# Optimization experiments

Hardware: AMD Instinct MI355X
Metric: run time of the kernel (lower is better)

Reference implementation:

```python
import jax, jax.numpy as jnp
import numpy as np

# dims: batch, n_sentences, n_comments, embedding_dim(==latent_dim), k
B, NS, NC, D, K = 16, 1024, 1024, 128, 128
K_CONV = 128.0   # curvature passed to poincare<->lorentz conversions (forward uses curv = self.k)
K_MAN = 1.0      # Lorentz manifold curvature (curv=1.0)
MIN_NORM = 1e-15


def p2l(x, k):
    # geoopt lmath.poincare_to_lorentz: dim d -> d+1
    x2 = jnp.sum(x * x, axis=-1, keepdims=True)
    return jnp.sqrt(k) * jnp.concatenate([1.0 + x2, 2.0 * x], axis=-1) / (1.0 - x2 + 1e-6)


def l2p(x, k):
    # geoopt lmath.lorentz_to_poincare: dim d+1 -> d
    return x[..., 1:] / (x[..., :1] + jnp.sqrt(k))


def lorentz_linear(x, W, b, log_scale):
    # HyboNet-style LorentzLinear: euclidean linear then rescale space so time^2 - |space|^2 = 1
    y = x @ W.T + b
    time = jax.nn.sigmoid(y[..., :1]) * jnp.exp(log_scale) + 1.1
    space = y[..., 1:]
    s2 = jnp.clip(jnp.sum(space * space, axis=-1, keepdims=True), 1e-8, None)
    return jnp.concatenate([time, space * jnp.sqrt((time * time - 1.0) / s2)], axis=-1)


def lorentz_tanh(x):
    # LorentzAct(tanh): tanh on space components, recompute time on the k=1 hyperboloid
    space = jnp.tanh(x[..., 1:])
    time = jnp.sqrt(K_MAN + jnp.sum(space * space, axis=-1, keepdims=True))
    return jnp.concatenate([time, space], axis=-1)


def artanh(x):
    return jnp.arctanh(jnp.clip(x, -1.0 + 1e-5, 1.0 - 1e-5))


def mobius_scale(mx, x_norm):
    # geoopt mobius_matvec (c=1) given the plain matrix product mx and the input row norms
    mx_norm = jnp.clip(jnp.linalg.norm(mx, axis=-1, keepdims=True), MIN_NORM, None)
    return jnp.tanh(mx_norm / x_norm * artanh(x_norm)) * mx / mx_norm


def mobius_add(x, y):
    # geoopt mobius_add, c=1
    xy = jnp.sum(x * y, axis=-1, keepdims=True)
    x2 = jnp.sum(x * x, axis=-1, keepdims=True)
    y2 = jnp.sum(y * y, axis=-1, keepdims=True)
    num = (1.0 + 2.0 * xy + y2) * x + (1.0 - x2) * y
    return num / jnp.clip(1.0 + 2.0 * xy + x2 * y2, MIN_NORM, None)


def lorentz_centroid(w, x):
    # CustomLorentz.centroid: weighted sum projected back to the hyperboloid
    avg = jnp.einsum('bqn,bnd->bqd', w, x)
    inner = jnp.sum(avg[..., 1:] ** 2, axis=-1, keepdims=True) - avg[..., :1] ** 2  # <avg,avg>_L
    return jnp.sqrt(K_MAN) * avg / jnp.sqrt(jnp.clip(jnp.abs(inner), 1e-8, None))


def setup_inputs() -> dict:
    key = jax.random.key(0)
    ks = jax.random.split(key, 8)

    def ball(k_, shape):
        # points safely inside the unit Poincare ball (norm ~ 0.58)
        u = jax.random.uniform(k_, shape, jnp.float32, minval=-1.0, maxval=1.0)
        return u / jnp.sqrt(jnp.float32(shape[-1]))

    def lin(k_, din, dout):
        kw, kb = jax.random.split(k_)
        W = jax.random.normal(kw, (dout, din), jnp.float32) * jnp.float32(1.0 / np.sqrt(din))
        b = jax.random.normal(kb, (dout,), jnp.float32) * 0.01
        return W, b

    Wl_w, Wl_b = lin(ks[2], D + 1, D + 1)
    Ws_w, Ws_b = lin(ks[3], D + 1, K + 1)
    Wc_w, Wc_b = lin(ks[4], D + 1, K + 1)
    return {
        'sentence_rep': ball(ks[0], (B, NS, D)),
        'comment_rep': ball(ks[1], (B, NC, D)),
        'Wl_w': Wl_w, 'Wl_b': Wl_b, 'Wl_scale': jnp.float32(np.log(10.0)),
        'Ws_w': Ws_w, 'Ws_b': Ws_b, 'Ws_scale': jnp.float32(np.log(10.0)),
        'Wc_w': Wc_w, 'Wc_b': Wc_b, 'Wc_scale': jnp.float32(np.log(10.0)),
        'whs': jax.random.normal(ks[5], (1, K + 1), jnp.float32),
        'whc': jax.random.normal(ks[6], (1, K + 1), jnp.float32),
    }


def reference(sentence_rep, comment_rep, Wl_w, Wl_b, Wl_scale, Ws_w, Ws_b, Ws_scale,
              Wc_w, Wc_b, Wc_scale, whs, whc):
    ls = p2l(sentence_rep, K_CONV)                       # [B,NS,D+1]
    lc = p2l(comment_rep, K_CONV)                        # [B,NC,D+1]

    Lw = lorentz_linear(lc, Wl_w, Wl_b, Wl_scale)        # [B,NC,D+1]
    L = lorentz_tanh(jnp.einsum('bsd,bcd->bsc', ls, Lw)) # [B,NS,NC] affinity

    Ps = l2p(lorentz_linear(ls, Ws_w, Ws_b, Ws_scale), K_CONV)  # [B,NS,K]
    Pc = l2p(lorentz_linear(lc, Wc_w, Wc_b, Wc_scale), K_CONV)  # [B,NC,K]

    Ln = jnp.clip(jnp.linalg.norm(L, axis=-1, keepdims=True), MIN_NORM, None)      # row norms of L
    LTn = jnp.clip(jnp.linalg.norm(L, axis=-2), MIN_NORM, None)[..., None]         # row norms of L^T

    Hs = lorentz_tanh(p2l(mobius_add(Ps, mobius_scale(jnp.einsum('bsc,bck->bsk', L, Pc), Ln)), K_CONV))   # [B,NS,K+1]
    Hc = lorentz_tanh(p2l(mobius_add(Pc, mobius_scale(jnp.einsum('bsc,bsk->bck', L, Ps), LTn)), K_CONV))  # [B,NC,K+1]

    Hs_n = jnp.clip(jnp.linalg.norm(Hs, axis=-1, keepdims=True), MIN_NORM, None)
    Hc_n = jnp.clip(jnp.linalg.norm(Hc, axis=-1, keepdims=True), MIN_NORM, None)
    As = jax.nn.softmax(mobius_scale(jnp.einsum('bnk,ok->bno', Hs, whs), Hs_n).swapaxes(-1, -2), axis=-1)  # [B,1,NS]
    Ac = jax.nn.softmax(mobius_scale(jnp.einsum('bnk,ok->bno', Hc, whc), Hc_n).swapaxes(-1, -2), axis=-1)  # [B,1,NC]

    co_s = lorentz_centroid(As, ls)                      # [B,1,D+1]
    co_c = lorentz_centroid(Ac, lc)                      # [B,1,D+1]

    # Lorentz direct concat: concat space parts, recompute time
    space = jnp.concatenate([co_s[..., 1:], co_c[..., 1:]], axis=-1)
    time = jnp.sqrt(K_MAN + jnp.sum(space * space, axis=-1, keepdims=True))
    co_sc = jnp.concatenate([time, space], axis=-1)[:, 0, :]  # squeeze -> [B,2D+1]
    return co_sc, As, Ac
```

## Files before the change

### kernel.cpp

```cpp
#include <hip/hip_runtime.h>

#define NN 1024
#define NB 16
#define SQRTK 11.313708498984761f

typedef float f32x4 __attribute__((ext_vector_type(4)));
typedef short bf16x8 __attribute__((ext_vector_type(8)));
typedef unsigned short ushort_t;
typedef unsigned int uint_t;

__device__ __forceinline__ ushort_t f2bf(float f){
  uint_t u = __float_as_uint(f);
  u += 0x7fffu + ((u>>16)&1u);
  return (ushort_t)(u>>16);
}
__device__ __forceinline__ float bf2f(ushort_t h){ return __uint_as_float(((uint_t)h)<<16); }

__device__ __forceinline__ uint_t cvtpk_bf16(float a, float b){
  uint_t r;
  asm("v_cvt_pk_bf16_f32 %0, %1, %2" : "=v"(r) : "v"(a), "v"(b));
  return r;
}

__device__ __forceinline__ float fast_tanh(float x){
  float e = __expf(2.f*x);
  return 1.f - 2.f/(e+1.f);
}

__device__ __forceinline__ float artanh_clip(float x){
  x = fminf(fmaxf(x, -1.0f+1e-5f), 1.0f-1e-5f);
  return 0.5f*__logf((1.0f+x)/(1.0f-x));
}

__device__ __forceinline__ void stage_swz(const ushort_t* __restrict__ g, int row_stride,
                                          char* ldsbase, int nrows, int tid, int nw){
  int lane = tid & 63;
  int w = tid >> 6;
  int ninst = nrows >> 2;
  int r_in = lane >> 4;
  int s_in = lane & 15;
  for (int inst = w; inst < ninst; inst += nw){
    int r = (inst<<2) + r_in;
    int s = s_in ^ (r & 15);
    const ushort_t* src = g + (size_t)r*row_stride + (s<<3);
    int instU = __builtin_amdgcn_readfirstlane(inst);
    __builtin_amdgcn_global_load_lds((const __attribute__((address_space(1))) void*)src,
        (__attribute__((address_space(3))) void*)(ldsbase + (instU<<10)), 16, 0, 0);
  }
}

__device__ __forceinline__ bf16x8 ldsfrag(const char* base, int r, int slot){
  return *(const bf16x8*)(base + ((r<<8) + ((slot ^ (r&15))<<4)));
}

__global__ void k_p2l(const float* __restrict__ S, const float* __restrict__ C,
                      ushort_t* __restrict__ lsb, ushort_t* __restrict__ lcb,
                      float* __restrict__ lst, float* __restrict__ lct,
                      const float* __restrict__ Wl, const float* __restrict__ Ws,
                      const float* __restrict__ Wc, ushort_t* __restrict__ Wb,
                      float* __restrict__ Wt){
  if (blockIdx.x >= 8192){
    int gid = (blockIdx.x - 8192)*256 + threadIdx.x;
    int w = gid / 18432;
    int rem = gid - w*18432;
    int j = rem >> 7, col = rem & 127;
    const float* W = (w==0)? Wl : (w==1? Ws : Wc);
    float v;
    if (j < 128) v = W[j*129 + 1 + col];
    else if (j == 128) v = W[128*129 + 1 + col];
    else v = 0.f;
    Wb[(size_t)w*18432 + (j<<7) + col] = f2bf(v);
    if (col==0 && j<=128) Wt[w*132 + j] = W[j*129];
    return;
  }
  int gr = (blockIdx.x<<2) + (threadIdx.x>>6);
  int lane = threadIdx.x & 63;
  const float* in; ushort_t* ob; float* ot;
  if (gr < (NB<<10)){ in = S + (size_t)gr*128; ob = lsb + (size_t)gr*128; ot = lst+gr; }
  else { int r = gr - (NB<<10); in = C + (size_t)r*128; ob = lcb + (size_t)r*128; ot = lct+r; }
  float2 v = ((const float2*)in)[lane];
  float sq = v.x*v.x + v.y*v.y;
  #pragma unroll
  for (int o=32;o>0;o>>=1) sq += __shfl_xor(sq, o, 64);
  float inv = SQRTK/(1.f - sq + 1e-6f);
  uint_t pack = (uint_t)f2bf(2.f*v.x*inv) | ((uint_t)f2bf(2.f*v.y*inv)<<16);
  ((uint_t*)ob)[lane] = pack;
  if (lane==0) *ot = (1.f+sq)*inv;
}

__global__ __launch_bounds__(256) void k_linf(
    const ushort_t* __restrict__ lsb, const ushort_t* __restrict__ lcb,
    const float* __restrict__ lst, const float* __restrict__ lct,
    const ushort_t* __restrict__ Wb, const float* __restrict__ Wt,
    const float* __restrict__ bl, const float* __restrict__ bs, const float* __restrict__ bc,
    const float* __restrict__ scl, const float* __restrict__ scs, const float* __restrict__ scc,
    ushort_t* __restrict__ Lwb, float* __restrict__ Lwt,
    ushort_t* __restrict__ Psb, ushort_t* __restrict__ Pcb,
    ushort_t* __restrict__ PsT, ushort_t* __restrict__ PcT){
  __shared__ __attribute__((aligned(1024))) char Al[16*1024];
  __shared__ __attribute__((aligned(1024))) char Bl[33*1024];
  __shared__ float XtF[64];
  __shared__ float wtsh[128];
  __shared__ float bsh[129];
  __shared__ float y128sh[64];
  __shared__ float y0sh[64];
  __shared__ float red2[64][2];
  __shared__ float facsh[64];
  int which = blockIdx.y;
  int m0 = blockIdx.x << 6;
  const ushort_t* A = ((which==1)? lsb : lcb) + (size_t)m0*128;
  const float* At = ((which==1)? lst : lct) + m0;
  const ushort_t* B = Wb + (size_t)which*18432;
  const float* bias = (which==0)? bl : (which==1? bs : bc);
  float scale = __expf((which==0)? *scl : (which==1? *scs : *scc));
  int tid = threadIdx.x, lane = tid&63, w = tid>>6;
  int wr = w>>1, wc = w&1, lo = lane&15, hi = lane>>4;
  stage_swz(A, 128, Al, 64, tid, 4);
  stage_swz(B, 128, Bl, 132, tid, 4);
  if (tid < 64) XtF[tid] = At[tid];
  if (tid < 128) wtsh[tid] = Wt[which*132 + tid];
  for (int i2 = tid; i2 < 129; i2 += 256) bsh[i2] = bias[i2];
  __syncthreads();
  f32x4 acc[2][4];
  f32x4 acc5[2];
  #pragma unroll
  for (int i=0;i<2;i++){
    acc5[i] = (f32x4){0.f,0.f,0.f,0.f};
    #pragma unroll
    for (int q=0;q<4;q++) acc[i][q] = (f32x4){0.f,0.f,0.f,0.f};
  }
  #pragma unroll
  for (int kc=0; kc<4; ++kc){
    bf16x8 av[2], bv[4];
    #pragma unroll
    for (int i=0;i<2;i++) av[i] = ldsfrag(Al, (wr<<5)+(i<<4)+lo, (kc<<2)+hi);
    #pragma unroll
    for (int q=0;q<4;q++) bv[q] = ldsfrag(Bl, (wc<<6)+(q<<4)+lo, (kc<<2)+hi);
    #pragma unroll
    for (int i=0;i<2;i++)
      #pragma unroll
      for (int q=0;q<4;q++)
        acc[i][q] = __builtin_amdgcn_mfma_f32_16x16x32_bf16(av[i], bv[q], acc[i][q], 0,0,0);
    if (wc==0){
      bf16x8 bv5 = ldsfrag(Bl, 128 + (lo&3), (kc<<2)+hi);
      #pragma unroll
      for (int i=0;i<2;i++)
        acc5[i] = __builtin_amdgcn_mfma_f32_16x16x32_bf16(av[i], bv5, acc5[i], 0,0,0);
    }
  }
  if (wc==0 && lo==0){
    #pragma unroll
    for (int i=0;i<2;i++)
      #pragma unroll
      for (int j=0;j<4;j++)
        y128sh[(wr<<5)+(i<<4)+(hi<<2)+j] = acc5[i][j];
  }
  float s2p[2][4];
  #pragma unroll
  for (int i=0;i<2;i++)
    #pragma unroll
    for (int j=0;j<4;j++) s2p[i][j] = 0.f;
  #pragma unroll
  for (int i=0;i<2;i++){
    f32x4 xt4 = *(const f32x4*)&XtF[(wr<<5)+(i<<4)+(hi<<2)];
    #pragma unroll
    for (int q=0;q<4;q++){
      int cl = (wc<<6)+(q<<4)+lo;
      float wtv = wtsh[cl];
      float bvv = bsh[cl];
      #pragma unroll
      for (int j=0;j<4;j++){
        float y = acc[i][q][j] + xt4[j]*wtv + bvv;
        acc[i][q][j] = y;
        if (cl==0){ y0sh[(wr<<5)+(i<<4)+(hi<<2)+j] = y; }
        else s2p[i][j] += y*y;
      }
    }
  }
  #pragma unroll
  for (int i=0;i<2;i++)
    #pragma unroll
    for (int j=0;j<4;j++){
      float v = s2p[i][j];
      v += __shfl_xor(v,1,64); v += __shfl_xor(v,2,64);
      v += __shfl_xor(v,4,64); v += __shfl_xor(v,8,64);
      s2p[i][j] = v;
    }
  if (lo==0){
    #pragma unroll
    for (int i=0;i<2;i++)
      #pragma unroll
      for (int j=0;j<4;j++) red2[(wr<<5)+(i<<4)+(hi<<2)+j][wc] = s2p[i][j];
  }
  __syncthreads();
  if (tid < 64){
    float wt128t = Wt[which*132 + 128];
    float y128v = y128sh[tid] + XtF[tid]*wt128t + bsh[128];
    y128sh[tid] = y128v;
    float s2 = fmaxf(red2[tid][0]+red2[tid][1] + y128v*y128v, 1e-8f);
    float y0 = y0sh[tid];
    float time = scale/(1.f+__expf(-y0)) + 1.1f;
    float fac = sqrtf((time*time-1.f)/s2);
    float iv = (which==0)? fac : fac/(time+SQRTK);
    facsh[tid] = iv;
    if (which==0) Lwt[m0+tid] = time;
  }
  __syncthreads();
  ushort_t* T2 = (ushort_t*)Bl;
  ushort_t* Ob = ((which==0)? Lwb : (which==1? Psb : Pcb)) + (size_t)m0*128;
  #pragma unroll
  for (int i=0;i<2;i++){
    f32x4 fv = *(const f32x4*)&facsh[(wr<<5)+(i<<4)+(hi<<2)];
    #pragma unroll
    for (int q=0;q<4;q++){
      int cl = (wc<<6)+(q<<4)+lo;
      if (cl > 0){
        #pragma unroll
        for (int j=0;j<4;j++){
          int row = (wr<<5)+(i<<4)+(hi<<2)+j;
          ushort_t v16 = f2bf(acc[i][q][j]*fv[j]);
          Ob[(size_t)row*128 + (cl-1)] = v16;
          if (which) T2[(cl-1)*68 + row] = v16;
        }
      }
    }
  }
  if (tid < 64){
    ushort_t v16 = f2bf(y128sh[tid]*facsh[tid]);
    Ob[(size_t)tid*128 + 127] = v16;
    if (which) T2[127*68 + tid] = v16;
  }
  if (which){
    __syncthreads();
    int b = m0 >> 10, n0 = m0 & 1023;
    ushort_t* PT = ((which==1)? PsT : PcT) + ((size_t)b<<17) + n0;
    for (int idx = tid; idx < 2048; idx += 256){
      int k = idx >> 4, seg = idx & 15;
      uint2 v = *(const uint2*)&T2[k*68 + (seg<<2)];
      *(uint2*)(PT + (size_t)k*1024 + (seg<<2)) = v;
    }
  }
}

__global__ __launch_bounds__(512) void k_fused(
    const ushort_t* __restrict__ lsb, const float* __restrict__ lst,
    const ushort_t* __restrict__ Lwb, const float* __restrict__ Lwt,
    const ushort_t* __restrict__ PsT, const ushort_t* __restrict__ PcT,
    const ushort_t* __restrict__ Pcb,
    float* __restrict__ mxs, float* __restrict__ mxc,
    float* __restrict__ Ln, float* __restrict__ LTn, float* __restrict__ tv){
  __shared__ __attribute__((aligned(1024))) char Rres[16*1024];
  __shared__ __attribute__((aligned(1024))) char STbuf[32*1024];
  __shared__ __attribute__((aligned(1024))) char Pbuf[16*1024];
  __shared__ float RtF[64];
  __shared__ float StF[128];
  __shared__ float pc0[128];
  __shared__ float red[64][4];
  __shared__ float tvsh[64];
  int side = blockIdx.y;
  int bx = blockIdx.x;
  bx = ((bx & 7) << 5) + (bx >> 3);
  int b = bx >> 4;
  int r0 = (bx & 15) << 6;
  const ushort_t* Rb = (side? Lwb : lsb) + ((size_t)((b<<10) + r0))*128;
  const float*    Rt = (side? Lwt : lst) + (b<<10) + r0;
  const ushort_t* Sb = (side? lsb : Lwb) + ((size_t)(b<<10))*128;
  const float*    St = (side? lst : Lwt) + (b<<10);
  const ushort_t* Tb = (side? PsT : PcT) + ((size_t)b<<17);
  float* C = (side? mxc : mxs) + ((size_t)((b<<10) + r0))*128;
  int tid = threadIdx.x, lane = tid&63, w = tid>>6;
  int lo = lane&15, hi = lane>>4;
  int wS = w>>1, wR = w&1;
  int wm = w&1, wn = w>>1;
  f32x4 acc2[2][2];
  #pragma unroll
  for (int i=0;i<2;i++)
    #pragma unroll
    for (int q=0;q<2;q++) acc2[i][q] = (f32x4){0.f,0.f,0.f,0.f};
  float tpart[2] = {0.f, 0.f};
  stage_swz(Rb, 128, Rres, 64, tid, 8);
  if (tid < 64) RtF[tid] = Rt[tid];
  if (tid < 128) pc0[tid] = side ? 0.f : bf2f(Pcb[((size_t)(b<<10))*128 + tid]);
  for (int ct=0; ct<8; ++ct){
    int s0 = ct<<7;
    __syncthreads();
    stage_swz(Sb + (size_t)s0*128, 128, STbuf, 128, tid, 8);
    if (tid < 128) StF[tid] = St[s0 + tid];
    __syncthreads();
    f32x4 d[2][2];
    #pragma unroll
    for (int i=0;i<2;i++)
      #pragma unroll
      for (int q=0;q<2;q++) d[i][q] = (f32x4){0.f,0.f,0.f,0.f};
    #pragma unroll
    for (int kc=0;kc<4;kc++){
      bf16x8 av[2], bv[2];
      #pragma unroll
      for (int i=0;i<2;i++) av[i] = ldsfrag(STbuf, (wS<<5)+(i<<4)+lo, (kc<<2)+hi);
      #pragma unroll
      for (int q=0;q<2;q++) bv[q] = ldsfrag(Rres, (wR<<5)+(q<<4)+lo, (kc<<2)+hi);
      #pragma unroll
      for (int i=0;i<2;i++)
        #pragma unroll
        for (int q=0;q<2;q++)
          d[i][q] = __builtin_amdgcn_mfma_f32_16x16x32_bf16(av[i], bv[q], d[i][q], 0,0,0);
    }
    __syncthreads();
    stage_swz(Tb + s0, 1024, STbuf, 128, tid, 8);
    #pragma unroll
    for (int i=0;i<2;i++){
      int st4 = (wS<<5)+(i<<4)+(hi<<2);
      f32x4 stv = *(const f32x4*)&StF[st4];
      #pragma unroll
      for (int q=0;q<2;q++){
        int rs = (wR<<5)+(q<<4)+lo;
        float rt = RtF[rs];
        float tval[4];
        #pragma unroll
        for (int j=0;j<4;j++){
          float val = d[i][q][j] + stv[j]*rt;
          bool dead = side ? ((r0+rs)==0) : ((s0+st4+j)==0);
          float tvv = fast_tanh(val);
          tvv = dead ? 0.f : tvv;
          tpart[q] += tvv*tvv;
          tval[j] = tvv;
        }
        uint2 pw;
        pw.x = cvtpk_bf16(tval[0], tval[1]);
        pw.y = cvtpk_bf16(tval[2], tval[3]);
        *(uint2*)(Pbuf + (rs<<8) + ((((st4>>3)^(rs&15)))<<4) + ((st4&7)<<1)) = pw;
      }
    }
    __syncthreads();
    #pragma unroll
    for (int kc=0;kc<4;kc++){
      bf16x8 av2[2], bv2[2];
      #pragma unroll
      for (int i=0;i<2;i++) av2[i] = ldsfrag(Pbuf, (wm<<5)+(i<<4)+lo, (kc<<2)+hi);
      #pragma unroll
      for (int q=0;q<2;q++) bv2[q] = ldsfrag(STbuf, (wn<<5)+(q<<4)+lo, (kc<<2)+hi);
      #pragma unroll
      for (int i=0;i<2;i++)
        #pragma unroll
        for (int q=0;q<2;q++)
          acc2[i][q] = __builtin_amdgcn_mfma_f32_16x16x32_bf16(av2[i], bv2[q], acc2[i][q], 0,0,0);
    }
  }
  #pragma unroll
  for (int q=0;q<2;q++){
    tpart[q] += __shfl_xor(tpart[q], 16, 64);
    tpart[q] += __shfl_xor(tpart[q], 32, 64);
  }
  if (hi==0){
    #pragma unroll
    for (int q=0;q<2;q++) red[(wR<<5)+(q<<4)+lo][w>>1] = tpart[q];
  }
  __syncthreads();
  if (tid < 64){
    float T = red[tid][0]+red[tid][1]+red[tid][2]+red[tid][3];
    int g = (b<<10) + r0 + tid;
    if (side==0){
      float timev = sqrtf(1.f+T);
      tvsh[tid] = timev;
      tv[g] = timev;
      Ln[g] = sqrtf(1.f+2.f*T);
    } else {
      if ((r0+tid) != 0) LTn[g] = fmaxf(sqrtf(T), 1e-15f);
      tvsh[tid] = 0.f;
    }
  }
  __syncthreads();
  #pragma unroll
  for (int i=0;i<2;i++){
    int rr4 = (wm<<5)+(i<<4)+(hi<<2);
    f32x4 tvv = *(const f32x4*)&tvsh[rr4];
    #pragma unroll
    for (int q=0;q<2;q++){
      int k = (wn<<5)+(q<<4)+lo;
      float p0 = pc0[k];
      #pragma unroll
      for (int j=0;j<4;j++){
        float v = acc2[i][q][j];
        if (side==0) v += tvv[j]*p0;
        C[(size_t)(rr4+j)*128 + k] = v;
      }
    }
  }
}

__global__ void k_fix2(const float* __restrict__ tv, const ushort_t* __restrict__ Psb,
                       float* __restrict__ mxc, float* __restrict__ LTn){
  __shared__ float tvl[1024];
  __shared__ float fpar[8][128];
  __shared__ float red16[16];
  int b = blockIdx.x, t = threadIdx.x;
  float v = tv[(b<<10)+t];
  tvl[t] = v;
  float sq = v*v;
  #pragma unroll
  for (int o=32;o>0;o>>=1) sq += __shfl_xor(sq,o,64);
  if ((t&63)==0) red16[t>>6] = sq;
  __syncthreads();
  int ch = t>>7, k = t&127;
  const ushort_t* P = Psb + (((size_t)(b<<10)) + (ch<<7))*128;
  const float* tc = &tvl[ch<<7];
  float acc = 0.f;
  #pragma unroll 4
  for (int s=0; s<128; ++s) acc += tc[s]*bf2f(P[(size_t)s*128 + k]);
  fpar[ch][k] = acc;
  __syncthreads();
  if (t < 128){
    float a = 0.f;
    #pragma unroll
    for (int c2=0; c2<8; ++c2) a += fpar[c2][t];
    mxc[((size_t)(b<<10))*128 + t] = a;
  }
  if (t == 0){
    float s = 0.f;
    #pragma unroll
    for (int c2=0; c2<16; ++c2) s += red16[c2];
    LTn[b<<10] = fmaxf(sqrtf(s), 1e-15f);
  }
}

__global__ __launch_bounds__(256) void k_epi(const float* __restrict__ mxs,
    const float* __restrict__ mxc,
    const ushort_t* __restrict__ Psb, const ushort_t* __restrict__ Pcb,
    const float* __restrict__ Ln, const float* __restrict__ LTn,
    const float* __restrict__ whs, const float* __restrict__ whc, float* __restrict__ logit){
  int wid = threadIdx.x >> 6, lane = threadIdx.x & 63;
  int gr = (blockIdx.x << 2) + wid;
  int side = gr >> 14, row = gr & 16383;
  const float* mx = (side? mxc : mxs) + (size_t)row*128;
  const ushort_t* xP = (side? Pcb : Psb) + (size_t)row*128;
  float xn = (side? LTn : Ln)[row];
  const float* wh = side? whc : whs;
  float2 mv = ((const float2*)mx)[lane];
  uint_t xu = ((const uint_t*)xP)[lane];
  float x0 = bf2f((ushort_t)(xu & 0xffffu));
  float x1 = bf2f((ushort_t)(xu >> 16));
  float pa = mv.x*mv.x + mv.y*mv.y;
  float pb = x0*x0 + x1*x1;
  float pc = x0*mv.x + x1*mv.y;
  #pragma unroll
  for (int o=32;o>0;o>>=1){
    pa += __shfl_xor(pa,o,64);
    pb += __shfl_xor(pb,o,64);
    pc += __shfl_xor(pc,o,64);
  }
  float mxn = fmaxf(sqrtf(pa), 1e-15f);
  float at1 = artanh_clip(xn);
  float fac = fast_tanh(mxn/xn*at1)/mxn;
  float xy = fac*pc;
  float x2 = pb;
  float y2 = fac*fac*pa;
  float den = fmaxf(1.0f + 2.0f*xy + x2*y2, 1e-15f);
  float ca = (1.0f+2.0f*xy+y2)/den;
  float cb = (1.0f-x2)*fac/den;
  float ma0 = ca*x0 + cb*mv.x;
  float ma1 = ca*x1 + cb*mv.y;
  float pm = ma0*ma0 + ma1*ma1;
  #pragma unroll
  for (int o=32;o>0;o>>=1) pm += __shfl_xor(pm,o,64);
  float scal = SQRTK*2.0f/(1.0f - pm + 1e-6f);
  float h0 = fast_tanh(scal*ma0);
  float h1 = fast_tanh(scal*ma1);
  float wv0 = wh[1 + 2*lane];
  float wv1 = wh[2 + 2*lane];
  float ps = h0*h0 + h1*h1;
  float pd = h0*wv0 + h1*wv1;
  #pragma unroll
  for (int o=32;o>0;o>>=1){
    ps += __shfl_xor(ps,o,64);
    pd += __shfl_xor(pd,o,64);
  }
  float timev = sqrtf(1.0f + ps);
  float hn = fmaxf(sqrtf(1.0f + 2.0f*ps), 1e-15f);
  float dotv = pd + timev*wh[0];
  float at2 = artanh_clip(hn);
  float mn = fmaxf(fabsf(dotv), 1e-15f);
  float lg = fast_tanh(mn/hn*at2)*(dotv/mn);
  if (lane==0) logit[gr] = lg;
}

__global__ void k_softmax(const float* __restrict__ logit,
                          float* __restrict__ outAs, float* __restrict__ outAc){
  __shared__ float red4[4];
  int side = blockIdx.x >> 4;
  int b = blockIdx.x & 15;
  const float* lg = logit + (side<<14) + (b<<10);
  float* out = (side? outAc : outAs) + (b<<10);
  int t = threadIdx.x;
  float l[4]; float m = -1e30f;
  #pragma unroll
  for (int i=0;i<4;i++){ l[i] = lg[t+256*i]; m = fmaxf(m,l[i]); }
  #pragma unroll
  for (int o=32;o>0;o>>=1) m = fmaxf(m, __shfl_xor(m,o,64));
  if ((t&63)==0) red4[t>>6]=m;
  __syncthreads();
  m = fmaxf(fmaxf(red4[0],red4[1]), fmaxf(red4[2],red4[3]));
  __syncthreads();
  float s = 0.f; float e[4];
  #pragma unroll
  for (int i=0;i<4;i++){ e[i] = __expf(l[i]-m); s += e[i]; }
  #pragma unroll
  for (int o=32;o>0;o>>=1) s += __shfl_xor(s,o,64);
  if ((t&63)==0) red4[t>>6]=s;
  __syncthreads();
  s = red4[0]+red4[1]+red4[2]+red4[3];
  float invs = 1.0f/s;
  #pragma unroll
  for (int i=0;i<4;i++) out[t+256*i] = e[i]*invs;
}

__global__ void k_cpart(const float* __restrict__ As0, const float* __restrict__ Ac0,
    const ushort_t* __restrict__ lsb, const ushort_t* __restrict__ lcb,
    const float* __restrict__ lst, const float* __restrict__ lct, float* __restrict__ part){
  __shared__ float Psh[64];
  __shared__ float ppar[128];
  int ch = blockIdx.x, b = blockIdx.y, side = blockIdx.z;
  const float* P = (side? Ac0 : As0) + (b<<10) + (ch<<6);
  const ushort_t* Xb = (side? lcb : lsb) + (((size_t)(b<<10)) + (ch<<6))*128;
  const float* Xt = (side? lct : lst) + (b<<10) + (ch<<6);
  int t = threadIdx.x;
  if (t < 64) Psh[t] = P[t];
  __syncthreads();
  int col = t & 127, half = t >> 7;
  float acc = 0.f;
  int n0 = half<<5;
  #pragma unroll 4
  for (int n=n0; n<n0+32; ++n) acc += Psh[n]*bf2f(Xb[(size_t)n*128 + col]);
  if (half==1) ppar[col] = acc;
  float acct = 0.f;
  if (t==255){
    for (int n=0;n<64;++n) acct += Psh[n]*Xt[n];
  }
  __syncthreads();
  size_t base = ((((size_t)side<<4) + b)*16 + ch)*132;
  if (t < 128) part[base + t] = acc + ppar[t];
  if (t == 255) part[base + 128] = acct;
}

__global__ void k_cfin2(const float* __restrict__ part, float* __restrict__ out){
  __shared__ float red4[4];
  __shared__ float t0sh;
  __shared__ float csh[2][128];
  int b = blockIdx.x, t = threadIdx.x;
  for (int side=0; side<2; ++side){
    int sb = side*16 + b;
    float a = 0.f;
    if (t <= 128){
      #pragma unroll
      for (int ch=0; ch<16; ++ch) a += part[((size_t)sb*16+ch)*132 + t];
    }
    float val = (t < 128)? a*a : 0.f;
    #pragma unroll
    for (int o=32;o>0;o>>=1) val += __shfl_xor(val,o,64);
    __syncthreads();
    if ((t&63)==0) red4[t>>6]=val;
    if (t==128) t0sh = a;
    __syncthreads();
    float S = red4[0]+red4[1]+red4[2]+red4[3];
    float timev = t0sh;
    float dn = sqrtf(fmaxf(fabsf(S - timev*timev), 1e-8f));
    if (t < 128) csh[side][t] = a/dn;
  }
  __syncthreads();
  float sp = (t<128)? csh[0][t] : csh[1][t-128];
  float v = sp*sp;
  #pragma unroll
  for (int o=32;o>0;o>>=1) v += __shfl_xor(v,o,64);
  __syncthreads();
  if ((t&63)==0) red4[t>>6]=v;
  __syncthreads();
  float S = red4[0]+red4[1]+red4[2]+red4[3];
  float* ob = out + (size_t)b*257;
  if (t==0) ob[0] = sqrtf(1.0f + S);
  ob[1+t] = sp;
}

extern "C" void kernel_launch(void* const* d_in, const int* in_sizes, int n_in,
                              void* d_out, int out_size, void* d_ws, size_t ws_size,
                              hipStream_t stream) {
  const float* srep = (const float*)d_in[0];
  const float* crep = (const float*)d_in[1];
  const float* Wl_w = (const float*)d_in[2];
  const float* Wl_b = (const float*)d_in[3];
  const float* Wl_s = (const float*)d_in[4];
  const float* Ws_w = (const float*)d_in[5];
  const float* Ws_b = (const float*)d_in[6];
  const float* Ws_s = (const float*)d_in[7];
  const float* Wc_w = (const float*)d_in[8];
  const float* Wc_b = (const float*)d_in[9];
  const float* Wc_s = (const float*)d_in[10];
  const float* whs  = (const float*)d_in[11];
  const float* whc  = (const float*)d_in[12];
  float* out = (float*)d_out;

  char* wsb = (char*)d_ws;
  size_t off = 0;
  auto alloc = [&](size_t n)->char*{ char* p = wsb + off; off += (n + 255) & ~(size_t)255; return p; };
  ushort_t* lsb = (ushort_t*)alloc((size_t)16384*128*2);
  ushort_t* lcb = (ushort_t*)alloc((size_t)16384*128*2);
  float* lst = (float*)alloc(16384*4);
  float* lct = (float*)alloc(16384*4);
  ushort_t* Wb = (ushort_t*)alloc((size_t)3*18432*2);
  float* Wt = (float*)alloc(3*132*4);
  ushort_t* Lwb = (ushort_t*)alloc((size_t)16384*128*2);
  float* Lwt = (float*)alloc(16384*4);
  ushort_t* Psb = (ushort_t*)alloc((size_t)16384*128*2);
  ushort_t* Pcb = (ushort_t*)alloc((size_t)16384*128*2);
  ushort_t* PsT = (ushort_t*)alloc((size_t)16*128*1024*2);
  ushort_t* PcT = (ushort_t*)alloc((size_t)16*128*1024*2);
  float* mxs = (float*)alloc((size_t)16384*128*4);
  float* mxc = (float*)alloc((size_t)16384*128*4);
  float* Ln = (float*)alloc(16384*4);
  float* LTn = (float*)alloc(16384*4);
  float* tv = (float*)alloc(16384*4);
  float* logit = (float*)alloc((size_t)2*16384*4);
  float* part = (float*)alloc((size_t)2*16*16*132*4);

  float* outAs = out + NB*257;
  float* outAc = out + NB*257 + NB*NN;

  k_p2l<<<8408, 256, 0, stream>>>(srep, crep, lsb, lcb, lst, lct,
                                  Wl_w, Ws_w, Wc_w, Wb, Wt);
  k_linf<<<dim3(256,3), 256, 0, stream>>>(lsb, lcb, lst, lct, Wb, Wt,
                                          Wl_b, Ws_b, Wc_b,
                                          Wl_s, Ws_s, Wc_s, Lwb, Lwt, Psb, Pcb,
                                          PsT, PcT);
  k_fused<<<dim3(256,2), 512, 0, stream>>>(lsb, lst, Lwb, Lwt, PsT, PcT, Pcb,
                                           mxs, mxc, Ln, LTn, tv);
  k_fix2<<<16, 1024, 0, stream>>>(tv, Psb, mxc, LTn);
  k_epi<<<8192, 256, 0, stream>>>(mxs, mxc, Psb, Pcb, Ln, LTn, whs, whc, logit);
  k_softmax<<<32, 256, 0, stream>>>(logit, outAs, outAc);
  k_cpart<<<dim3(16,16,2), 256, 0, stream>>>(outAs, outAc, lsb, lcb, lst, lct, part);
  k_cfin2<<<16, 256, 0, stream>>>(part, out);
}
```

Baseline: 105.1 us.

## Fuse Poincare-to-Lorentz conversion into linear kernel and fix-up into epilogue

Removes the standalone p2l kernel: k_linf now loads fp32 inputs and weights directly, computes the Lorentz conversion and bf16 packing in registers, writes swizzled tiles to LDS, and stores lsb/lcb for later use. The k_fix2 kernel is folded into k_epi as 16 extra blocks that compute the row-0 comment correction and its logit directly. This cuts two launches and the intermediate round trip through global memory, at the cost of redundant weight conversion per block and a serial 512-step loop in the extra blocks that may lengthen the epilogue's tail. Which=0 (Wl path) reads C and writes lct, which appears to rely on the lcb/lct layout convention.

```diff
diff --git a/kernel.cpp b/kernel.cpp
--- a/kernel.cpp
+++ b/kernel.cpp
@@ -53,45 +53,11 @@
   return *(const bf16x8*)(base + ((r<<8) + ((slot ^ (r&15))<<4)));
 }
 
-__global__ void k_p2l(const float* __restrict__ S, const float* __restrict__ C,
-                      ushort_t* __restrict__ lsb, ushort_t* __restrict__ lcb,
-                      float* __restrict__ lst, float* __restrict__ lct,
-                      const float* __restrict__ Wl, const float* __restrict__ Ws,
-                      const float* __restrict__ Wc, ushort_t* __restrict__ Wb,
-                      float* __restrict__ Wt){
-  if (blockIdx.x >= 8192){
-    int gid = (blockIdx.x - 8192)*256 + threadIdx.x;
-    int w = gid / 18432;
-    int rem = gid - w*18432;
-    int j = rem >> 7, col = rem & 127;
-    const float* W = (w==0)? Wl : (w==1? Ws : Wc);
-    float v;
-    if (j < 128) v = W[j*129 + 1 + col];
-    else if (j == 128) v = W[128*129 + 1 + col];
-    else v = 0.f;
-    Wb[(size_t)w*18432 + (j<<7) + col] = f2bf(v);
-    if (col==0 && j<=128) Wt[w*132 + j] = W[j*129];
-    return;
-  }
-  int gr = (blockIdx.x<<2) + (threadIdx.x>>6);
-  int lane = threadIdx.x & 63;
-  const float* in; ushort_t* ob; float* ot;
-  if (gr < (NB<<10)){ in = S + (size_t)gr*128; ob = lsb + (size_t)gr*128; ot = lst+gr; }
-  else { int r = gr - (NB<<10); in = C + (size_t)r*128; ob = lcb + (size_t)r*128; ot = lct+r; }
-  float2 v = ((const float2*)in)[lane];
-  float sq = v.x*v.x + v.y*v.y;
-  #pragma unroll
-  for (int o=32;o>0;o>>=1) sq += __shfl_xor(sq, o, 64);
-  float inv = SQRTK/(1.f - sq + 1e-6f);
-  uint_t pack = (uint_t)f2bf(2.f*v.x*inv) | ((uint_t)f2bf(2.f*v.y*inv)<<16);
-  ((uint_t*)ob)[lane] = pack;
-  if (lane==0) *ot = (1.f+sq)*inv;
-}
-
 __global__ __launch_bounds__(256) void k_linf(
-    const ushort_t* __restrict__ lsb, const ushort_t* __restrict__ lcb,
-    const float* __restrict__ lst, const float* __restrict__ lct,
-    const ushort_t* __restrict__ Wb, const float* __restrict__ Wt,
+    const float* __restrict__ S, const float* __restrict__ C,
+    ushort_t* __restrict__ lsb, ushort_t* __restrict__ lcb,
+    float* __restrict__ lst, float* __restrict__ lct,
+    const float* __restrict__ Wl, const float* __restrict__ Ws, const float* __restrict__ Wc,
     const float* __restrict__ bl, const float* __restrict__ bs, const float* __restrict__ bc,
     const float* __restrict__ scl, const float* __restrict__ scs, const float* __restrict__ scc,
     ushort_t* __restrict__ Lwb, float* __restrict__ Lwt,
@@ -108,18 +74,85 @@
   __shared__ float facsh[64];
   int which = blockIdx.y;
   int m0 = blockIdx.x << 6;
-  const ushort_t* A = ((which==1)? lsb : lcb) + (size_t)m0*128;
-  const float* At = ((which==1)? lst : lct) + m0;
-  const ushort_t* B = Wb + (size_t)which*18432;
+  const float* X = (which==1)? S : C;
+  const float* W = (which==0)? Wl : (which==1? Ws : Wc);
   const float* bias = (which==0)? bl : (which==1? bs : bc);
   float scale = __expf((which==0)? *scl : (which==1? *scs : *scc));
   int tid = threadIdx.x, lane = tid&63, w = tid>>6;
   int wr = w>>1, wc = w&1, lo = lane&15, hi = lane>>4;
-  stage_swz(A, 128, Al, 64, tid, 4);
-  stage_swz(B, 128, Bl, 132, tid, 4);
-  if (tid < 64) XtF[tid] = At[tid];
-  if (tid < 128) wtsh[tid] = Wt[which*132 + tid];
-  for (int i2 = tid; i2 < 129; i2 += 256) bsh[i2] = bias[i2];
+
+  {
+    int r = tid>>2, q = tid&3;
+    const float* src = X + (size_t)(m0+r)*128 + (q<<5);
+    float4 xv[8];
+    #pragma unroll
+    for (int u=0;u<8;u++) xv[u] = ((const float4*)src)[u];
+    float sq = 0.f;
+    #pragma unroll
+    for (int u=0;u<8;u++) sq += xv[u].x*xv[u].x + xv[u].y*xv[u].y + xv[u].z*xv[u].z + xv[u].w*xv[u].w;
+    sq += __shfl_xor(sq,1,64);
+    sq += __shfl_xor(sq,2,64);
+    float inv = SQRTK/(1.f - sq + 1e-6f);
+    uint_t pk[16];
+    #pragma unroll
+    for (int u=0;u<8;u++){
+      pk[2*u]   = (uint_t)f2bf(2.f*xv[u].x*inv) | ((uint_t)f2bf(2.f*xv[u].y*inv)<<16);
+      pk[2*u+1] = (uint_t)f2bf(2.f*xv[u].z*inv) | ((uint_t)f2bf(2.f*xv[u].w*inv)<<16);
+    }
+    #pragma unroll
+    for (int u4=0; u4<4; ++u4){
+      int slog = (q<<2)+u4;
+      *(uint4*)(Al + (r<<8) + ((slog ^ (r&15))<<4)) =
+          make_uint4(pk[4*u4], pk[4*u4+1], pk[4*u4+2], pk[4*u4+3]);
+    }
+    if (which != 2){
+      ushort_t* gdst = ((which==1)? lsb : lcb) + ((size_t)(m0+r)<<7) + (q<<5);
+      #pragma unroll
+      for (int u4=0; u4<4; ++u4)
+        ((uint4*)gdst)[u4] = make_uint4(pk[4*u4], pk[4*u4+1], pk[4*u4+2], pk[4*u4+3]);
+    }
+    float timev = (1.f+sq)*inv;
+    if (q==0){
+      XtF[r] = timev;
+      if (which==1) lst[m0+r] = timev;
+      else if (which==0) lct[m0+r] = timev;
+    }
+  }
+  {
+    int j = tid>>1, h = tid&1;
+    const float* wrow = W + (size_t)j*129 + 1 + (h<<6);
+    #pragma unroll
+    for (int u8=0; u8<8; ++u8){
+      uint_t wp[4];
+      #pragma unroll
+      for (int p2=0; p2<4; ++p2){
+        float a = wrow[u8*8 + 2*p2];
+        float b2 = wrow[u8*8 + 2*p2 + 1];
+        wp[p2] = (uint_t)f2bf(a) | ((uint_t)f2bf(b2)<<16);
+      }
+      int slog = (h<<3)+u8;
+      *(uint4*)(Bl + (j<<8) + ((slog ^ (j&15))<<4)) = make_uint4(wp[0],wp[1],wp[2],wp[3]);
+    }
+    if (tid < 8){
+      int jr = 128 + (tid>>1), hh = tid&1;
+      #pragma unroll
+      for (int u8=0; u8<8; ++u8){
+        uint_t wp[4] = {0u,0u,0u,0u};
+        if (jr == 128){
+          #pragma unroll
+          for (int p2=0; p2<4; ++p2){
+            float a = W[(size_t)128*129 + 1 + (hh<<6) + u8*8 + 2*p2];
+            float b2 = W[(size_t)128*129 + 1 + (hh<<6) + u8*8 + 2*p2 + 1];
+            wp[p2] = (uint_t)f2bf(a) | ((uint_t)f2bf(b2)<<16);
+          }
+        }
+        int slog = (hh<<3)+u8;
+        *(uint4*)(Bl + (jr<<8) + ((slog ^ (jr&15))<<4)) = make_uint4(wp[0],wp[1],wp[2],wp[3]);
+      }
+    }
+    if (tid < 128) wtsh[tid] = W[(size_t)tid*129];
+    for (int i2 = tid; i2 < 129; i2 += 256) bsh[i2] = bias[i2];
+  }
   __syncthreads();
   f32x4 acc[2][4];
   f32x4 acc5[2];
@@ -194,7 +227,7 @@
   }
   __syncthreads();
   if (tid < 64){
-    float wt128t = Wt[which*132 + 128];
+    float wt128t = W[(size_t)128*129];
     float y128v = y128sh[tid] + XtF[tid]*wt128t + bsh[128];
     y128sh[tid] = y128v;
     float s2 = fmaxf(red2[tid][0]+red2[tid][1] + y128v*y128v, 1e-8f);
@@ -388,46 +421,83 @@
   }
 }
 
-__global__ void k_fix2(const float* __restrict__ tv, const ushort_t* __restrict__ Psb,
-                       float* __restrict__ mxc, float* __restrict__ LTn){
-  __shared__ float tvl[1024];
-  __shared__ float fpar[8][128];
-  __shared__ float red16[16];
-  int b = blockIdx.x, t = threadIdx.x;
-  float v = tv[(b<<10)+t];
-  tvl[t] = v;
-  float sq = v*v;
-  #pragma unroll
-  for (int o=32;o>0;o>>=1) sq += __shfl_xor(sq,o,64);
-  if ((t&63)==0) red16[t>>6] = sq;
-  __syncthreads();
-  int ch = t>>7, k = t&127;
-  const ushort_t* P = Psb + (((size_t)(b<<10)) + (ch<<7))*128;
-  const float* tc = &tvl[ch<<7];
-  float acc = 0.f;
-  #pragma unroll 4
-  for (int s=0; s<128; ++s) acc += tc[s]*bf2f(P[(size_t)s*128 + k]);
-  fpar[ch][k] = acc;
-  __syncthreads();
-  if (t < 128){
-    float a = 0.f;
-    #pragma unroll
-    for (int c2=0; c2<8; ++c2) a += fpar[c2][t];
-    mxc[((size_t)(b<<10))*128 + t] = a;
-  }
-  if (t == 0){
-    float s = 0.f;
-    #pragma unroll
-    for (int c2=0; c2<16; ++c2) s += red16[c2];
-    LTn[b<<10] = fmaxf(sqrtf(s), 1e-15f);
-  }
-}
-
 __global__ __launch_bounds__(256) void k_epi(const float* __restrict__ mxs,
     const float* __restrict__ mxc,
     const ushort_t* __restrict__ Psb, const ushort_t* __restrict__ Pcb,
     const float* __restrict__ Ln, const float* __restrict__ LTn,
-    const float* __restrict__ whs, const float* __restrict__ whc, float* __restrict__ logit){
+    const float* __restrict__ whs, const float* __restrict__ whc,
+    const float* __restrict__ tv, float* __restrict__ logit){
+  if (blockIdx.x >= 8192){
+    __shared__ float tvl[1024];
+    __shared__ float mx0[2][128];
+    __shared__ float redf[4];
+    int b = blockIdx.x - 8192, t = threadIdx.x, lane = t&63;
+    float4 tva = ((const float4*)(tv + (b<<10)))[t];
+    *(float4*)&tvl[t<<2] = tva;
+    float sq = tva.x*tva.x + tva.y*tva.y + tva.z*tva.z + tva.w*tva.w;
+    #pragma unroll
+    for (int o=32;o>0;o>>=1) sq += __shfl_xor(sq,o,64);
+    if (lane==0) redf[t>>6] = sq;
+    int k = t&127, h = t>>7;
+    const ushort_t* P = Psb + ((size_t)((b<<10) + (h<<9)))*128 + k;
+    const float* tc = &tvl[h<<9];
+    float acc = 0.f;
+    #pragma unroll 8
+    for (int s=0; s<512; ++s) acc += tc[s]*bf2f(P[(size_t)s*128]);
+    mx0[h][k] = acc;
+    __syncthreads();
+    if (t < 64){
+      float xn = fmaxf(sqrtf(redf[0]+redf[1]+redf[2]+redf[3]), 1e-15f);
+      float2 mv = { mx0[0][2*lane] + mx0[1][2*lane],
+                    mx0[0][2*lane+1] + mx0[1][2*lane+1] };
+      uint_t xu = ((const uint_t*)(Pcb + ((size_t)(b<<10))*128))[lane];
+      float x0 = bf2f((ushort_t)(xu & 0xffffu));
+      float x1 = bf2f((ushort_t)(xu >> 16));
+      float pa = mv.x*mv.x + mv.y*mv.y;
+      float pb = x0*x0 + x1*x1;
+      float pc = x0*mv.x + x1*mv.y;
+      #pragma unroll
+      for (int o=32;o>0;o>>=1){
+        pa += __shfl_xor(pa,o,64);
+        pb += __shfl_xor(pb,o,64);
+        pc += __shfl_xor(pc,o,64);
+      }
+      float mxn = fmaxf(sqrtf(pa), 1e-15f);
+      float at1 = artanh_clip(xn);
+      float fac = fast_tanh(mxn/xn*at1)/mxn;
+      float xy = fac*pc;
+      float x2 = pb;
+      float y2 = fac*fac*pa;
+      float den = fmaxf(1.0f + 2.0f*xy + x2*y2, 1e-15f);
+      float ca = (1.0f+2.0f*xy+y2)/den;
+      float cb = (1.0f-x2)*fac/den;
+      float ma0 = ca*x0 + cb*mv.x;
+      float ma1 = ca*x1 + cb*mv.y;
+      float pm = ma0*ma0 + ma1*ma1;
+      #pragma unroll
+      for (int o=32;o>0;o>>=1) pm += __shfl_xor(pm,o,64);
+      float scal = SQRTK*2.0f/(1.0f - pm + 1e-6f);
+      float h0 = fast_tanh(scal*ma0);
+      float h1 = fast_tanh(scal*ma1);
+      float wv0 = whc[1 + 2*lane];
+      float wv1 = whc[2 + 2*lane];
+      float ps = h0*h0 + h1*h1;
+      float pd = h0*wv0 + h1*wv1;
+      #pragma unroll
+      for (int o=32;o>0;o>>=1){
+        ps += __shfl_xor(ps,o,64);
+        pd += __shfl_xor(pd,o,64);
+      }
+      float timev = sqrtf(1.0f + ps);
+      float hn = fmaxf(sqrtf(1.0f + 2.0f*ps), 1e-15f);
+      float dotv = pd + timev*whc[0];
+      float at2 = artanh_clip(hn);
+      float mn = fmaxf(fabsf(dotv), 1e-15f);
+      float lg = fast_tanh(mn/hn*at2)*(dotv/mn);
+      if (lane==0) logit[(1<<14)+(b<<10)] = lg;
+    }
+    return;
+  }
   int wid = threadIdx.x >> 6, lane = threadIdx.x & 63;
   int gr = (blockIdx.x << 2) + wid;
   int side = gr >> 14, row = gr & 16383;
@@ -480,7 +550,9 @@
   float at2 = artanh_clip(hn);
   float mn = fmaxf(fabsf(dotv), 1e-15f);
   float lg = fast_tanh(mn/hn*at2)*(dotv/mn);
-  if (lane==0) logit[gr] = lg;
+  if (lane==0 && !((side==1) && ((row & 1023)==0) && (row>>10)>=0 && row==( (row>>10)<<10 ))){
+  }
+  if (lane==0 && !((side==1) && ((row & 1023)==0))) logit[gr] = lg;
 }
 
 __global__ void k_softmax(const float* __restrict__ logit,
@@ -604,8 +676,6 @@
   ushort_t* lcb = (ushort_t*)alloc((size_t)16384*128*2);
   float* lst = (float*)alloc(16384*4);
   float* lct = (float*)alloc(16384*4);
-  ushort_t* Wb = (ushort_t*)alloc((size_t)3*18432*2);
-  float* Wt = (float*)alloc(3*132*4);
   ushort_t* Lwb = (ushort_t*)alloc((size_t)16384*128*2);
   float* Lwt = (float*)alloc(16384*4);
   ushort_t* Psb = (ushort_t*)alloc((size_t)16384*128*2);
@@ -623,16 +693,13 @@
   float* outAs = out + NB*257;
   float* outAc = out + NB*257 + NB*NN;
 
-  k_p2l<<<8408, 256, 0, stream>>>(srep, crep, lsb, lcb, lst, lct,
-                                  Wl_w, Ws_w, Wc_w, Wb, Wt);
-  k_linf<<<dim3(256,3), 256, 0, stream>>>(lsb, lcb, lst, lct, Wb, Wt,
-                                          Wl_b, Ws_b, Wc_b,
+  k_linf<<<dim3(256,3), 256, 0, stream>>>(srep, crep, lsb, lcb, lst, lct,
+                                          Wl_w, Ws_w, Wc_w, Wl_b, Ws_b, Wc_b,
                                           Wl_s, Ws_s, Wc_s, Lwb, Lwt, Psb, Pcb,
                                           PsT, PcT);
   k_fused<<<dim3(256,2), 512, 0, stream>>>(lsb, lst, Lwb, Lwt, PsT, PcT, Pcb,
                                            mxs, mxc, Ln, LTn, tv);
-  k_fix2<<<16, 1024, 0, stream>>>(tv, Psb, mxc, LTn);
-  k_epi<<<8192, 256, 0, stream>>>(mxs, mxc, Psb, Pcb, Ln, LTn, whs, whc, logit);
+  k_epi<<<8208, 256, 0, stream>>>(mxs, mxc, Psb, Pcb, Ln, LTn, whs, whc, tv, logit);
   k_softmax<<<32, 256, 0, stream>>>(logit, outAs, outAc);
   k_cpart<<<dim3(16,16,2), 256, 0, stream>>>(outAs, outAc, lsb, lcb, lst, lct, part);
   k_cfin2<<<16, 256, 0, stream>>>(part, out);
```

New measurement: 111.3 us. 5.9% more time.
